# Optimization experiments

Measured on AMD Instinct MI355X. Metric: run time of the kernel, lower is better.

## Reference

```python
import jax, jax.numpy as jnp
import numpy as np
from jax.scipy.linalg import solve_triangular

NUM_EMBEDDINGS = 512
EMBEDDING_DIM = 64
SPARSITY = 5
COMMITMENT_COST = 0.25


def batch_omp(data, dictionary, max_nonzero):
    """Batch OMP. data: (M, B), dictionary: (M, N). Returns coeffs (N, B)."""
    M, B = data.shape
    Dt = dictionary.T                       # (N, M)
    G = Dt @ dictionary                     # (N, N) Gram matrix
    h_bar = (Dt @ data).T                   # (B, N)
    h = h_bar
    x = jnp.zeros_like(h_bar)               # (B, N)
    L = jnp.ones((B, 1, 1), data.dtype)     # growing Cholesky factor
    mask = jnp.zeros(h_bar.shape, dtype=bool)
    I = None                                # selected atom indices (B, k)
    bidx = jnp.arange(B)
    for k in range(1, max_nonzero + 1):     # small fixed unroll (5 iters)
        index = jnp.argmax(jnp.abs(h * (~mask)), axis=1)   # (B,)
        mask = mask.at[bidx, index].set(True)
        if k > 1:
            # G[I_b, index_b] for each batch element -> (B, k-1, 1)
            G_stack = G[I, index[:, None]][..., None]
            w = solve_triangular(L, G_stack, lower=True)   # (B, k-1, 1)
            wT = jnp.swapaxes(w, 1, 2)                     # (B, 1, k-1)
            w_corner = jnp.sqrt(jnp.clip(1.0 - jnp.sum(wT ** 2, axis=2, keepdims=True), 0.0))
            top = jnp.concatenate([L, jnp.zeros((B, k - 1, 1), L.dtype)], axis=2)
            bot = jnp.concatenate([wT, w_corner], axis=2)
            L = jnp.concatenate([top, bot], axis=1)        # (B, k, k)
            I = jnp.concatenate([I, index[:, None]], axis=1)
        else:
            I = index[:, None]
        h_stack = jnp.take_along_axis(h_bar, I, axis=1)[..., None]  # (B, k, 1)
        y = solve_triangular(L, h_stack, lower=True)
        x_stack = solve_triangular(jnp.swapaxes(L, 1, 2), y, lower=False)  # (B, k, 1)
        x = x.at[bidx[:, None], I].set(x_stack[..., 0])
        beta = jnp.einsum('bk,bkn->bn', x_stack[..., 0], G[I])  # (B, N)
        h = h_bar - beta
    return x.T                              # (N, B)


def setup_inputs() -> dict:
    key = jax.random.key(0)
    k1, k2 = jax.random.split(key)
    z_e = jax.random.normal(k1, (32, EMBEDDING_DIM, 32, 32), dtype=jnp.float32)
    D = jax.random.normal(k2, (EMBEDDING_DIM, NUM_EMBEDDINGS), dtype=jnp.float32)
    D = D / jnp.linalg.norm(D, axis=0)      # column-normalized atoms (as _normalize_dictionary)
    return {"z_e": z_e, "dictionary": D}


def reference(z_e, dictionary):
    # permute BCHW -> BHWC, then flat view to (embedding_dim, -1) row-major (as torch .view)
    z_perm = jnp.transpose(z_e, (0, 2, 3, 1))          # (B, H, W, C)
    input_shape = z_perm.shape
    ze_flat = z_perm.reshape(EMBEDDING_DIM, -1)        # (M, Btokens)
    coefficients = batch_omp(ze_flat, dictionary, SPARSITY)  # (N, Btokens)
    z_dl = (dictionary @ coefficients).reshape(input_shape)
    e_latent_loss = jnp.mean((jax.lax.stop_gradient(z_dl) - z_perm) ** 2)
    dl_latent_loss = jnp.mean((z_dl - jax.lax.stop_gradient(z_perm)) ** 2)
    loss = COMMITMENT_COST * e_latent_loss + dl_latent_loss
    z_out = z_perm + jax.lax.stop_gradient(z_dl - z_perm)   # straight-through
    return (jnp.transpose(z_out, (0, 3, 1, 2)), loss, coefficients)
```

## Files before the change

### kernel.cpp

```cpp
#include <hip/hip_runtime.h>

#define B_TOTAL 32768
#define NATOM   512
#define MDIM    64
#define KS      5

__global__ void k_prep(const float* __restrict__ ze, float* __restrict__ dT,
                       const float* __restrict__ D, float* __restrict__ G,
                       float* __restrict__ acc, float4* __restrict__ coeff4) {
    __shared__ float lds[64][65];
    const int t = threadIdx.x;
    if (blockIdx.x < 512) {
        const int n   = blockIdx.x >> 4;
        const int hw0 = (blockIdx.x & 15) * 64;
#pragma unroll
        for (int r = 0; r < 16; ++r) {
            int id = r * 256 + t;
            int c = id >> 6, i = id & 63;
            lds[c][i] = ze[n * 65536 + c * 1024 + hw0 + i];
        }
        __syncthreads();
#pragma unroll
        for (int r = 0; r < 16; ++r) {
            int id = r * 256 + t;
            int c = id & 63, j = id >> 6;
            int hw = hw0 + j;
            int h = hw >> 5, w = hw & 31;
            int m = (n << 1) | (h >> 4);
            int b = ((h & 15) << 11) | (w << 6) | c;
            dT[m * 32768 + b] = lds[c][j];
        }
    } else if (blockIdx.x < 1024) {
        const int i = blockIdx.x - 512;
        float* col = &lds[0][0];
        if (t < MDIM) col[t] = D[t * NATOM + i];
        __syncthreads();
        for (int j = t; j < NATOM; j += 256) {
            float s = 0.f;
#pragma unroll
            for (int m = 0; m < MDIM; ++m) s = fmaf(col[m], D[m * NATOM + j], s);
            G[i * NATOM + j] = s;
        }
        if (i == 0 && t == 0) *acc = 0.f;
    } else {
        const int base = (blockIdx.x - 1024) * 4096;
        const float4 z = make_float4(0.f, 0.f, 0.f, 0.f);
#pragma unroll
        for (int r = 0; r < 16; ++r)
            coeff4[base + r * 256 + t] = z;
    }
}

__launch_bounds__(256, 2)
__global__ void k_omp(const float* __restrict__ data, const float* __restrict__ D,
                      const float* __restrict__ G, int* __restrict__ idx_out,
                      float* __restrict__ val_out) {
    const int t    = threadIdx.x;
    const int lane = t & 63;
    const int wv   = t >> 6;
    const int b0   = blockIdx.x * 32;

    __shared__ __align__(16) float data_s[32][68];
    __shared__ __align__(16) float stage[4][2048];

#pragma unroll
    for (int r = 0; r < 8; ++r) {
        int id = r * 256 + t;
        int m = id >> 5, bb = id & 31;
        data_s[bb][m] = data[m * B_TOTAL + b0 + bb];
    }
    __syncthreads();

    const float4* __restrict__ D4 = (const float4*)D;
    const float4* __restrict__ G4 = (const float4*)G;

    float4 acc[8][2];
#pragma unroll
    for (int bb = 0; bb < 8; ++bb) {
        acc[bb][0] = make_float4(0.f, 0.f, 0.f, 0.f);
        acc[bb][1] = make_float4(0.f, 0.f, 0.f, 0.f);
    }
    const int bwbase = wv * 8;

#pragma unroll 4
    for (int c = 0; c < 16; ++c) {
        float4 df[4][2];
#pragma unroll
        for (int mm = 0; mm < 4; ++mm) {
            df[mm][0] = D4[(c * 4 + mm) * 128 + lane];
            df[mm][1] = D4[(c * 4 + mm) * 128 + 64 + lane];
        }
#pragma unroll
        for (int bb = 0; bb < 8; ++bb) {
            const float4 dv = *(const float4*)&data_s[bwbase + bb][c * 4];
            const float dm[4] = {dv.x, dv.y, dv.z, dv.w};
#pragma unroll
            for (int mm = 0; mm < 4; ++mm) {
                acc[bb][0].x = fmaf(df[mm][0].x, dm[mm], acc[bb][0].x);
                acc[bb][0].y = fmaf(df[mm][0].y, dm[mm], acc[bb][0].y);
                acc[bb][0].z = fmaf(df[mm][0].z, dm[mm], acc[bb][0].z);
                acc[bb][0].w = fmaf(df[mm][0].w, dm[mm], acc[bb][0].w);
                acc[bb][1].x = fmaf(df[mm][1].x, dm[mm], acc[bb][1].x);
                acc[bb][1].y = fmaf(df[mm][1].y, dm[mm], acc[bb][1].y);
                acc[bb][1].z = fmaf(df[mm][1].z, dm[mm], acc[bb][1].z);
                acc[bb][1].w = fmaf(df[mm][1].w, dm[mm], acc[bb][1].w);
            }
        }
    }

    const int g = lane >> 3;
    const int p = lane & 7;
    float hb[64];
#pragma unroll
    for (int r = 0; r < 2; ++r) {
        __syncthreads();
#pragma unroll
        for (int q2 = 0; q2 < 4; ++q2) {
            int bb = r * 4 + q2;
            *(float4*)&stage[wv][q2 * 512 + 4 * lane]       = acc[bb][0];
            *(float4*)&stage[wv][q2 * 512 + 256 + 4 * lane] = acc[bb][1];
        }
        __syncthreads();
        if ((g >> 2) == r) {
#pragma unroll
            for (int q = 0; q < 16; ++q) {
                const float4 v =
                    *(const float4*)&stage[wv][(g & 3) * 512 + 32 * q + 4 * p];
                hb[4 * q + 0] = v.x;
                hb[4 * q + 1] = v.y;
                hb[4 * q + 2] = v.z;
                hb[4 * q + 3] = v.w;
            }
        }
    }

    float key[64];
#pragma unroll
    for (int e = 0; e < 64; ++e) key[e] = fabsf(hb[e]);

    unsigned msk0 = 0u, msk1 = 0u;
    int   I[KS];
    float xs[KS];
    float gsel[KS];
    float Lm[15];

#pragma unroll
    for (int k = 0; k < KS; ++k) {
        float cv[4]; int ce[4]; float ch[4];
#pragma unroll
        for (int c4 = 0; c4 < 4; ++c4) {
            cv[c4] = key[16 * c4]; ce[c4] = 16 * c4; ch[c4] = hb[16 * c4];
#pragma unroll
            for (int e = 16 * c4 + 1; e < 16 * c4 + 16; ++e) {
                bool gt = key[e] > cv[c4];
                cv[c4] = gt ? key[e] : cv[c4];
                ce[c4] = gt ? e      : ce[c4];
                ch[c4] = gt ? hb[e]  : ch[c4];
            }
        }
        float bv = cv[0]; int be = ce[0]; float bhb = ch[0];
#pragma unroll
        for (int c4 = 1; c4 < 4; ++c4) {
            bool gt = cv[c4] > bv;
            bv  = gt ? cv[c4] : bv;
            be  = gt ? ce[c4] : be;
            bhb = gt ? ch[c4] : bhb;
        }
        int bn = 32 * (be >> 2) + 4 * p + (be & 3);
#pragma unroll
        for (int off = 1; off < 8; off <<= 1) {
            float ov  = __shfl_xor(bv, off);
            int   on  = __shfl_xor(bn, off);
            float ohb = __shfl_xor(bhb, off);
            bool take = (ov > bv) || (ov == bv && on < bn);
            bv = take ? ov : bv; bn = take ? on : bn; bhb = take ? ohb : bhb;
        }
        const int nsel = bn;
        I[k]    = nsel;
        gsel[k] = bhb;

        {
            int own  = (nsel >> 2) & 7;
            int esel = ((nsel >> 5) << 2) | (nsel & 3);
            if (p == own) {
                if (esel < 32) msk0 |= 1u << esel;
                else           msk1 |= 1u << (esel - 32);
            }
        }

        if (k > 0) {
            float gk[KS - 1], w[KS - 1];
#pragma unroll
            for (int ti = 0; ti < KS - 1; ++ti)
                if (ti < k) gk[ti] = G[I[ti] * NATOM + nsel];
#pragma unroll
            for (int r = 0; r < KS - 1; ++r) {
                if (r < k) {
                    float s = gk[r];
#pragma unroll
                    for (int cc = 0; cc < KS - 1; ++cc)
                        if (cc < r) s -= Lm[r * (r + 1) / 2 + cc] * w[cc];
                    w[r] = s / Lm[r * (r + 1) / 2 + r];
                }
            }
            float s2 = 0.f;
#pragma unroll
            for (int r = 0; r < KS - 1; ++r) if (r < k) s2 += w[r] * w[r];
            float wc = sqrtf(fmaxf(0.f, 1.f - s2));
#pragma unroll
            for (int cc = 0; cc < KS - 1; ++cc)
                if (cc < k) Lm[k * (k + 1) / 2 + cc] = w[cc];
            Lm[k * (k + 1) / 2 + k] = wc;
        } else {
            Lm[0] = 1.f;
        }

        float y[KS];
#pragma unroll
        for (int r = 0; r <= k; ++r) {
            float s = gsel[r];
#pragma unroll
            for (int cc = 0; cc < r; ++cc) s -= Lm[r * (r + 1) / 2 + cc] * y[cc];
            y[r] = s / Lm[r * (r + 1) / 2 + r];
        }
#pragma unroll
        for (int r = k; r >= 0; --r) {
            float s = y[r];
#pragma unroll
            for (int cc = r + 1; cc <= k; ++cc) s -= Lm[cc * (cc + 1) / 2 + r] * xs[cc];
            xs[r] = s / Lm[r * (r + 1) / 2 + r];
        }

        if (k < KS - 1) {
#pragma unroll
            for (int q = 0; q < 16; ++q) {
                float bx = 0.f, by = 0.f, bz = 0.f, bw = 0.f;
#pragma unroll
                for (int ti = 0; ti < KS - 1; ++ti) {
                    if (ti <= k) {
                        const float4 gc = G4[I[ti] * 128 + 8 * q + p];
                        bx = fmaf(xs[ti], gc.x, bx);
                        by = fmaf(xs[ti], gc.y, by);
                        bz = fmaf(xs[ti], gc.z, bz);
                        bw = fmaf(xs[ti], gc.w, bw);
                    }
                }
                {
                    float d0 = hb[4 * q + 0] - bx;
                    float d1 = hb[4 * q + 1] - by;
                    float d2 = hb[4 * q + 2] - bz;
                    float d3 = hb[4 * q + 3] - bw;
                    const int e0 = 4 * q;
                    bool m0 = (e0 + 0 < 32) ? ((msk0 >> (e0 + 0)) & 1u) : ((msk1 >> (e0 - 32)) & 1u);
                    bool m1 = (e0 + 1 < 32) ? ((msk0 >> (e0 + 1)) & 1u) : ((msk1 >> (e0 + 1 - 32)) & 1u);
                    bool m2 = (e0 + 2 < 32) ? ((msk0 >> (e0 + 2)) & 1u) : ((msk1 >> (e0 + 2 - 32)) & 1u);
                    bool m3 = (e0 + 3 < 32) ? ((msk0 >> (e0 + 3)) & 1u) : ((msk1 >> (e0 + 3 - 32)) & 1u);
                    key[e0 + 0] = m0 ? -1.f : fabsf(d0);
                    key[e0 + 1] = m1 ? -1.f : fabsf(d1);
                    key[e0 + 2] = m2 ? -1.f : fabsf(d2);
                    key[e0 + 3] = m3 ? -1.f : fabsf(d3);
                }
            }
        }
    }

    if (p == 0) {
#pragma unroll
        for (int k = 0; k < KS; ++k) {
            idx_out[k * B_TOTAL + b0 + wv * 8 + g] = I[k];
            val_out[k * B_TOTAL + b0 + wv * 8 + g] = xs[k];
        }
    }
}

__global__ void k_post(const int* __restrict__ idx, const float* __restrict__ val,
                       float* __restrict__ coeff, const float* __restrict__ dataT,
                       const float* __restrict__ D, float* __restrict__ zout,
                       float* __restrict__ acc) {
    const int t = threadIdx.x;
    if (blockIdx.x < 128) {
        const int b = blockIdx.x * 256 + t;
#pragma unroll
        for (int k = 0; k < KS; ++k) {
            int   a = idx[k * B_TOTAL + b];
            float v = val[k * B_TOTAL + b];
            coeff[a * B_TOTAL + b] = v;
        }
    } else {
        __shared__ float lds[64][65];
        const int blk = blockIdx.x - 128;
        const int n   = blk >> 4;
        const int hw0 = (blk & 15) * 64;
        float sq = 0.f;
#pragma unroll
        for (int r = 0; r < 16; ++r) {
            int id = r * 256 + t;
            int c = id & 63, j = id >> 6;
            int f = n * 65536 + (hw0 + j) * 64 + c;
            int b = f & 32767;
            int m = f >> 15;
            float zdl = 0.f;
#pragma unroll
            for (int k = 0; k < KS; ++k) {
                int   a = idx[k * B_TOTAL + b];
                float v = val[k * B_TOTAL + b];
                zdl = fmaf(v, D[m * NATOM + a], zdl);
            }
            float zp   = dataT[f];
            float diff = zdl - zp;
            lds[c][j] = zp + diff;
            sq = fmaf(diff, diff, sq);
        }
        __syncthreads();
#pragma unroll
        for (int r = 0; r < 16; ++r) {
            int id = r * 256 + t;
            int cc = id >> 6, i = id & 63;
            zout[n * 65536 + cc * 1024 + hw0 + i] = lds[cc][i];
        }
#pragma unroll
        for (int off = 32; off > 0; off >>= 1) sq += __shfl_xor(sq, off);
        __shared__ float red[4];
        if ((t & 63) == 0) red[t >> 6] = sq;
        __syncthreads();
        if (t == 0) atomicAdd(acc, red[0] + red[1] + red[2] + red[3]);
    }
}

__global__ void k_loss(const float* __restrict__ acc, float* __restrict__ out_loss) {
    if (threadIdx.x == 0 && blockIdx.x == 0)
        *out_loss = 1.25f * (*acc / 2097152.f);
}

extern "C" void kernel_launch(void* const* d_in, const int* in_sizes, int n_in,
                              void* d_out, int out_size, void* d_ws, size_t ws_size,
                              hipStream_t stream) {
    const float* ze = (const float*)d_in[0];
    const float* D  = (const float*)d_in[1];

    float* G     = (float*)d_ws;
    int*   idxp  = (int*)  ((char*)d_ws + (size_t)262144 * 4);
    float* valp  = (float*)((char*)d_ws + (size_t)(262144 + 163840) * 4);
    float* accp  = (float*)((char*)d_ws + (size_t)(262144 + 2 * 163840) * 4);
    float* dataT = (float*)((char*)d_ws + (size_t)(262144 + 2 * 163840 + 64) * 4);

    float* zout  = (float*)d_out;
    float* lossp = zout + 2097152;
    float* coeff = zout + 2097153;

    k_prep<<<2048, 256, 0, stream>>>(ze, dataT, D, G, accp, (float4*)coeff);
    k_omp <<<1024, 256, 0, stream>>>(dataT, D, G, idxp, valp);
    k_post<<< 640, 256, 0, stream>>>(idxp, valp, coeff, dataT, D, zout, accp);
    k_loss<<<1, 64, 0, stream>>>(accp, lossp);
}
```

Before: 198.0 us.

## Write dense coefficients from OMP kernel and fold loss finalize into post

The separate zero-fill of the 512x32768 coefficient matrix in the prep kernel and the scatter pass in the post kernel are removed. Each OMP block now stages its selected indices and values in shared memory and writes its dense coefficient columns directly with float4 stores. The standalone loss kernel is replaced by a last-block-done counter in the post kernel, which computes the final loss. This removes one full pass of writes over the large coefficient buffer and one kernel launch. In exchange, the OMP kernel's tail gets longer and gains an extra barrier.

```diff
diff --git a/kernel.cpp b/kernel.cpp
--- a/kernel.cpp
+++ b/kernel.cpp
@@ -7,7 +7,7 @@
 
 __global__ void k_prep(const float* __restrict__ ze, float* __restrict__ dT,
                        const float* __restrict__ D, float* __restrict__ G,
-                       float* __restrict__ acc, float4* __restrict__ coeff4) {
+                       float* __restrict__ acc) {
     __shared__ float lds[64][65];
     const int t = threadIdx.x;
     if (blockIdx.x < 512) {
@@ -30,7 +30,7 @@
             int b = ((h & 15) << 11) | (w << 6) | c;
             dT[m * 32768 + b] = lds[c][j];
         }
-    } else if (blockIdx.x < 1024) {
+    } else {
         const int i = blockIdx.x - 512;
         float* col = &lds[0][0];
         if (t < MDIM) col[t] = D[t * NATOM + i];
@@ -41,20 +41,14 @@
             for (int m = 0; m < MDIM; ++m) s = fmaf(col[m], D[m * NATOM + j], s);
             G[i * NATOM + j] = s;
         }
-        if (i == 0 && t == 0) *acc = 0.f;
-    } else {
-        const int base = (blockIdx.x - 1024) * 4096;
-        const float4 z = make_float4(0.f, 0.f, 0.f, 0.f);
-#pragma unroll
-        for (int r = 0; r < 16; ++r)
-            coeff4[base + r * 256 + t] = z;
+        if (i == 0 && t == 0) { acc[0] = 0.f; ((unsigned*)acc)[1] = 0u; }
     }
 }
 
 __launch_bounds__(256, 2)
 __global__ void k_omp(const float* __restrict__ data, const float* __restrict__ D,
                       const float* __restrict__ G, int* __restrict__ idx_out,
-                      float* __restrict__ val_out) {
+                      float* __restrict__ val_out, float* __restrict__ coeff) {
     const int t    = threadIdx.x;
     const int lane = t & 63;
     const int wv   = t >> 6;
@@ -62,6 +56,8 @@
 
     __shared__ __align__(16) float data_s[32][68];
     __shared__ __align__(16) float stage[4][2048];
+    __shared__ int   idx_s[KS][32];
+    __shared__ float val_s[KS][32];
 
 #pragma unroll
     for (int r = 0; r < 8; ++r) {
@@ -267,69 +263,91 @@
     if (p == 0) {
 #pragma unroll
         for (int k = 0; k < KS; ++k) {
+            idx_s[k][wv * 8 + g] = I[k];
+            val_s[k][wv * 8 + g] = xs[k];
             idx_out[k * B_TOTAL + b0 + wv * 8 + g] = I[k];
             val_out[k * B_TOTAL + b0 + wv * 8 + g] = xs[k];
         }
     }
+    __syncthreads();
+
+    {
+        const int bq = t & 7;
+        const int jr = t >> 3;
+        int   Ib[4][KS]; float Vb[4][KS];
+#pragma unroll
+        for (int u = 0; u < 4; ++u)
+#pragma unroll
+            for (int k = 0; k < KS; ++k) {
+                Ib[u][k] = idx_s[k][bq * 4 + u];
+                Vb[u][k] = val_s[k][bq * 4 + u];
+            }
+#pragma unroll
+        for (int jj = 0; jj < 16; ++jj) {
+            const int j = jj * 32 + jr;
+            float w0 = 0.f, w1 = 0.f, w2 = 0.f, w3 = 0.f;
+#pragma unroll
+            for (int k = 0; k < KS; ++k) {
+                w0 = (Ib[0][k] == j) ? Vb[0][k] : w0;
+                w1 = (Ib[1][k] == j) ? Vb[1][k] : w1;
+                w2 = (Ib[2][k] == j) ? Vb[2][k] : w2;
+                w3 = (Ib[3][k] == j) ? Vb[3][k] : w3;
+            }
+            *(float4*)&coeff[(size_t)j * B_TOTAL + b0 + bq * 4] =
+                make_float4(w0, w1, w2, w3);
+        }
+    }
 }
 
 __global__ void k_post(const int* __restrict__ idx, const float* __restrict__ val,
-                       float* __restrict__ coeff, const float* __restrict__ dataT,
-                       const float* __restrict__ D, float* __restrict__ zout,
-                       float* __restrict__ acc) {
-    const int t = threadIdx.x;
-    if (blockIdx.x < 128) {
-        const int b = blockIdx.x * 256 + t;
+                       const float* __restrict__ dataT, const float* __restrict__ D,
+                       float* __restrict__ zout, float* __restrict__ acc,
+                       float* __restrict__ out_loss) {
+    __shared__ float lds[64][65];
+    const int t   = threadIdx.x;
+    const int n   = blockIdx.x >> 4;
+    const int hw0 = (blockIdx.x & 15) * 64;
+    float sq = 0.f;
+#pragma unroll
+    for (int r = 0; r < 16; ++r) {
+        int id = r * 256 + t;
+        int c = id & 63, j = id >> 6;
+        int f = n * 65536 + (hw0 + j) * 64 + c;
+        int b = f & 32767;
+        int m = f >> 15;
+        float zdl = 0.f;
 #pragma unroll
         for (int k = 0; k < KS; ++k) {
             int   a = idx[k * B_TOTAL + b];
             float v = val[k * B_TOTAL + b];
-            coeff[a * B_TOTAL + b] = v;
-        }
-    } else {
-        __shared__ float lds[64][65];
-        const int blk = blockIdx.x - 128;
-        const int n   = blk >> 4;
-        const int hw0 = (blk & 15) * 64;
-        float sq = 0.f;
-#pragma unroll
-        for (int r = 0; r < 16; ++r) {
-            int id = r * 256 + t;
-            int c = id & 63, j = id >> 6;
-            int f = n * 65536 + (hw0 + j) * 64 + c;
-            int b = f & 32767;
-            int m = f >> 15;
-            float zdl = 0.f;
-#pragma unroll
-            for (int k = 0; k < KS; ++k) {
-                int   a = idx[k * B_TOTAL + b];
-                float v = val[k * B_TOTAL + b];
-                zdl = fmaf(v, D[m * NATOM + a], zdl);
-            }
-            float zp   = dataT[f];
-            float diff = zdl - zp;
-            lds[c][j] = zp + diff;
-            sq = fmaf(diff, diff, sq);
-        }
-        __syncthreads();
-#pragma unroll
-        for (int r = 0; r < 16; ++r) {
-            int id = r * 256 + t;
-            int cc = id >> 6, i = id & 63;
-            zout[n * 65536 + cc * 1024 + hw0 + i] = lds[cc][i];
-        }
-#pragma unroll
-        for (int off = 32; off > 0; off >>= 1) sq += __shfl_xor(sq, off);
-        __shared__ float red[4];
-        if ((t & 63) == 0) red[t >> 6] = sq;
-        __syncthreads();
-        if (t == 0) atomicAdd(acc, red[0] + red[1] + red[2] + red[3]);
-    }
-}
-
-__global__ void k_loss(const float* __restrict__ acc, float* __restrict__ out_loss) {
-    if (threadIdx.x == 0 && blockIdx.x == 0)
-        *out_loss = 1.25f * (*acc / 2097152.f);
+            zdl = fmaf(v, D[m * NATOM + a], zdl);
+        }
+        float zp   = dataT[f];
+        float diff = zdl - zp;
+        lds[c][j] = zp + diff;
+        sq = fmaf(diff, diff, sq);
+    }
+    __syncthreads();
+#pragma unroll
+    for (int r = 0; r < 16; ++r) {
+        int id = r * 256 + t;
+        int cc = id >> 6, i = id & 63;
+        zout[n * 65536 + cc * 1024 + hw0 + i] = lds[cc][i];
+    }
+#pragma unroll
+    for (int off = 32; off > 0; off >>= 1) sq += __shfl_xor(sq, off);
+    __shared__ float red[4];
+    if ((t & 63) == 0) red[t >> 6] = sq;
+    __syncthreads();
+    if (t == 0) {
+        atomicAdd(acc, red[0] + red[1] + red[2] + red[3]);
+        __threadfence();
+        unsigned prev = atomicAdd(((unsigned*)acc) + 1, 1u);
+        if (prev == 511u) {
+            float a = atomicAdd(acc, 0.f);
+            out_loss[0] = 1.25f * (a / 2097152.f);
+        }
+    }
 }
 
 extern "C" void kernel_launch(void* const* d_in, const int* in_sizes, int n_in,
@@ -348,8 +366,7 @@
     float* lossp = zout + 2097152;
     float* coeff = zout + 2097153;
 
-    k_prep<<<2048, 256, 0, stream>>>(ze, dataT, D, G, accp, (float4*)coeff);
-    k_omp <<<1024, 256, 0, stream>>>(dataT, D, G, idxp, valp);
-    k_post<<< 640, 256, 0, stream>>>(idxp, valp, coeff, dataT, D, zout, accp);
-    k_loss<<<1, 64, 0, stream>>>(accp, lossp);
+    k_prep<<<1024, 256, 0, stream>>>(ze, dataT, D, G, accp);
+    k_omp <<<1024, 256, 0, stream>>>(dataT, D, G, idxp, valp, coeff);
+    k_post<<< 512, 256, 0, stream>>>(idxp, valp, dataT, D, zout, accp, lossp);
 }
```

New measurement: 200.2 us. About the same (+1.1%).
